# Performance work log

Hardware: AMD Instinct MI355X
Metric: run time of the kernel (lower is better)

The kernel has to match this reference:

```python
import jax, jax.numpy as jnp
import numpy as np

EMBED = 512
HEADS = 8
SCALE = 4
B, N = 2, 2048
DH = EMBED // HEADS
EPS = 1e-5


def _mha(q_in, k_in, v_in, wq, bq, wk, bk, wv, bv, wo, bo, causal):
    Bq, Nq, _ = q_in.shape
    Nk = k_in.shape[1]
    Q = (q_in @ wq + bq).reshape(Bq, Nq, HEADS, DH)
    K = (k_in @ wk + bk).reshape(Bq, Nk, HEADS, DH)
    V = (v_in @ wv + bv).reshape(Bq, Nk, HEADS, DH)
    # scores: [B, H, Nq, Nk]
    scores = jnp.einsum('bqhd,bkhd->bhqk', Q, K) / np.sqrt(DH).astype(np.float32)
    if causal:
        mask = jnp.triu(jnp.full((Nq, Nq), -jnp.inf, dtype=scores.dtype), k=1)
        scores = scores + mask[None, None]
    attn = jax.nn.softmax(scores, axis=-1)
    out = jnp.einsum('bhqk,bkhd->bqhd', attn, V).reshape(Bq, Nq, EMBED)
    return out @ wo + bo


def _ln(x, g, b):
    mu = jnp.mean(x, axis=-1, keepdims=True)
    var = jnp.var(x, axis=-1, keepdims=True)
    return (x - mu) * jax.lax.rsqrt(var + EPS) * g + b


def setup_inputs() -> dict:
    key = jax.random.key(0)
    ks = iter(jax.random.split(key, 32))
    p = lambda *s: 0.02 * jax.random.normal(next(ks), s, dtype=jnp.float32)
    inp = {
        'x': jax.random.normal(next(ks), (B, N, EMBED), dtype=jnp.float32),
        'encoder_output': jax.random.normal(next(ks), (B, N, EMBED), dtype=jnp.float32),
    }
    for pre in ('sa', 'ca'):
        inp[pre + '_wq'] = p(EMBED, EMBED); inp[pre + '_bq'] = jnp.zeros(EMBED)
        inp[pre + '_wk'] = p(EMBED, EMBED); inp[pre + '_bk'] = jnp.zeros(EMBED)
        inp[pre + '_wv'] = p(EMBED, EMBED); inp[pre + '_bv'] = jnp.zeros(EMBED)
        inp[pre + '_wo'] = p(EMBED, EMBED); inp[pre + '_bo'] = jnp.zeros(EMBED)
    for i in (1, 2, 3):
        inp[f'ln{i}_g'] = jnp.ones(EMBED); inp[f'ln{i}_b'] = jnp.zeros(EMBED)
    inp['ff_w1'] = p(EMBED, SCALE * EMBED); inp['ff_b1'] = jnp.zeros(SCALE * EMBED)
    inp['ff_w2'] = p(SCALE * EMBED, EMBED); inp['ff_b2'] = jnp.zeros(EMBED)
    return inp


def reference(x, encoder_output,
              sa_wq, sa_bq, sa_wk, sa_bk, sa_wv, sa_bv, sa_wo, sa_bo,
              ca_wq, ca_bq, ca_wk, ca_bk, ca_wv, ca_bv, ca_wo, ca_bo,
              ln1_g, ln1_b, ln2_g, ln2_b, ln3_g, ln3_b,
              ff_w1, ff_b1, ff_w2, ff_b2):
    x = _mha(x, x, x, sa_wq, sa_bq, sa_wk, sa_bk, sa_wv, sa_bv, sa_wo, sa_bo, True) + x
    x = _ln(x, ln1_g, ln1_b)
    x = _mha(x, encoder_output, encoder_output,
             ca_wq, ca_bq, ca_wk, ca_bk, ca_wv, ca_bv, ca_wo, ca_bo, False) + x
    x = _ln(x, ln2_g, ln2_b)
    h = jax.nn.gelu(x @ ff_w1 + ff_b1, approximate=False)
    x = h @ ff_w2 + ff_b2 + x
    return _ln(x, ln3_g, ln3_b)
```

## Files before the change

### kernel.cpp

```cpp
#include <hip/hip_runtime.h>
#include <hip/hip_bf16.h>

typedef __bf16 bf16x8 __attribute__((ext_vector_type(8)));
typedef float f32x4 __attribute__((ext_vector_type(4)));
typedef unsigned short u16;

#define EMB 512
#define FF 2048
#define MTOT 4096
#define SEQ 2048

__device__ __forceinline__ u16 f2b(float f) {
  return __builtin_bit_cast(u16, (__bf16)f);
}

__device__ __forceinline__ void gload16(const u16* g, u16* l) {
  __builtin_amdgcn_global_load_lds(
      (const __attribute__((address_space(1))) unsigned int*)g,
      (__attribute__((address_space(3))) unsigned int*)l, 16, 0, 0);
}

__global__ __launch_bounds__(256) void prep_all(
    const float* s0, const float* s1, const float* s2, const float* s3,
    const float* s4, const float* s5, const float* s6, const float* s7,
    const float* s8, const float* s9,
    u16* d0, u16* d1, u16* d2, u16* d3, u16* d4,
    u16* d5, u16* d6, u16* d7, u16* d8, u16* d9,
    const float* x, u16* xb, const float* enc, u16* encb,
    const float* bq1, const float* bk1, const float* bv1, float* bqkv,
    const float* bk2, const float* bv2, float* bkv) {
  int z = blockIdx.z, bx = blockIdx.x, by = blockIdx.y;
  int tid = threadIdx.x;
  if (z >= 10) {
    int fb = by * 64 + bx;
    const float* src = (z == 10) ? x : enc;
    u16* dst = (z == 10) ? xb : encb;
    size_t base = (size_t)fb * 2048 + tid * 8;
    float4 a = *(const float4*)(src + base);
    float4 b = *(const float4*)(src + base + 4);
    uint4 u;
    u.x = f2b(a.x) | ((unsigned)f2b(a.y) << 16);
    u.y = f2b(a.z) | ((unsigned)f2b(a.w) << 16);
    u.z = f2b(b.x) | ((unsigned)f2b(b.y) << 16);
    u.w = f2b(b.z) | ((unsigned)f2b(b.w) << 16);
    *(uint4*)(dst + base) = u;
    return;
  }
  if (z == 0 && bx == 16 && by == 0) {
    for (int i = tid; i < 1536; i += 256)
      bqkv[i] = (i < 512) ? bq1[i] : (i < 1024 ? bk1[i - 512] : bv1[i - 1024]);
    return;
  }
  if (z == 1 && bx == 16 && by == 0) {
    for (int i = tid; i < 1024; i += 256)
      bkv[i] = (i < 512) ? bk2[i] : bv2[i - 512];
    return;
  }
  const float* src; u16* dst; int K, N;
  switch (z) {
    case 0: src = s0; dst = d0; K = 512; N = 512; break;
    case 1: src = s1; dst = d1; K = 512; N = 512; break;
    case 2: src = s2; dst = d2; K = 512; N = 512; break;
    case 3: src = s3; dst = d3; K = 512; N = 512; break;
    case 4: src = s4; dst = d4; K = 512; N = 512; break;
    case 5: src = s5; dst = d5; K = 512; N = 512; break;
    case 6: src = s6; dst = d6; K = 512; N = 512; break;
    case 7: src = s7; dst = d7; K = 512; N = 512; break;
    case 8: src = s8; dst = d8; K = 512; N = 2048; break;
    default: src = s9; dst = d9; K = 2048; N = 512; break;
  }
  int ntl, ktl;
  if (z == 9) { ktl = bx; ntl = by; } else { ntl = bx; ktl = by; }
  if (ntl * 32 >= N || ktl * 32 >= K) return;
  __shared__ float t[32][33];
  int tx = tid & 31, ty = tid >> 5;
  int n0 = ntl * 32, k0 = ktl * 32;
#pragma unroll
  for (int i = 0; i < 4; i++)
    t[ty + i * 8][tx] = src[(size_t)(k0 + ty + i * 8) * N + n0 + tx];
  __syncthreads();
#pragma unroll
  for (int i = 0; i < 4; i++)
    dst[(size_t)(n0 + ty + i * 8) * K + k0 + tx] = f2b(t[tx][ty + i * 8]);
}

template <int BM, int BN, bool OUTB, bool OUTF, bool RES, bool GELU_>
__global__ __launch_bounds__(256) void gemm_bt(
    const u16* __restrict__ A, const u16* __restrict__ Bt,
    const float* __restrict__ bias, const float* __restrict__ resid,
    u16* __restrict__ outb, float* __restrict__ outf, int K, int Nd) {
  constexpr int MI = BM / 32;
  constexpr int NI = BN / 32;
  constexpr int RA = BM / 64;
  constexpr int RB = BN / 64;
  __shared__ u16 As[2][BM * 32];
  __shared__ u16 Bs[2][BN * 32];
  int tid = threadIdx.x;
  int lane = tid & 63, w = tid >> 6;
  int g = lane >> 4, li = lane & 15;
  int wr = w >> 1, wc = w & 1;
  int m0 = blockIdx.x * BM, n0 = blockIdx.y * BN;
  const u16* srcs[RA + RB];
  int ldsoff[RA + RB];
#pragma unroll
  for (int r = 0; r < RA + RB; r++) {
    int ca = (r < RA ? r * 256 : (r - RA) * 256) + tid;
    int row = ca >> 2, chv = ca & 3;
    int csw = chv ^ ((row ^ (row >> 2)) & 3);
    srcs[r] = (r < RA ? A + (size_t)(m0 + row) * K : Bt + (size_t)(n0 + row) * K) + csw * 8;
    ldsoff[r] = ((r < RA ? r * 256 : (r - RA) * 256) + w * 64) * 8;
  }
  int s2a = (li ^ (li >> 2)) & 3;
  f32x4 acc[MI][NI] = {};
  int T = K >> 5;
  auto stage = [&](int t, int buf) {
    int k0 = t << 5;
#pragma unroll
    for (int r = 0; r < RA; r++) gload16(srcs[r] + k0, &As[buf][ldsoff[r]]);
#pragma unroll
    for (int r = RA; r < RA + RB; r++) gload16(srcs[r] + k0, &Bs[buf][ldsoff[r]]);
  };
  stage(0, 0);
  __syncthreads();
  for (int t = 0; t < T; t++) {
    int cur = t & 1;
    if (t + 1 < T) stage(t + 1, cur ^ 1);
    bf16x8 af[MI], bfr[NI];
#pragma unroll
    for (int i = 0; i < MI; i++)
      af[i] = *(const bf16x8*)&As[cur][(wr * (BM / 2) + i * 16 + li) * 32 + (g ^ s2a) * 8];
#pragma unroll
    for (int i = 0; i < NI; i++)
      bfr[i] = *(const bf16x8*)&Bs[cur][(wc * (BN / 2) + i * 16 + li) * 32 + (g ^ s2a) * 8];
#pragma unroll
    for (int mi = 0; mi < MI; mi++)
#pragma unroll
      for (int ni = 0; ni < NI; ni++)
        acc[mi][ni] = __builtin_amdgcn_mfma_f32_16x16x32_bf16(af[mi], bfr[ni], acc[mi][ni], 0, 0, 0);
    __syncthreads();
  }
#pragma unroll
  for (int mi = 0; mi < MI; mi++)
#pragma unroll
    for (int ni = 0; ni < NI; ni++) {
      int gn = n0 + wc * (BN / 2) + ni * 16 + li;
      float bv = bias[gn];
#pragma unroll
      for (int r = 0; r < 4; r++) {
        int gm = m0 + wr * (BM / 2) + mi * 16 + g * 4 + r;
        float v = acc[mi][ni][r] + bv;
        if (RES) v += resid[(size_t)gm * Nd + gn];
        if (GELU_) v = 0.5f * v * (1.0f + erff(v * 0.70710678118654752f));
        if (OUTF) outf[(size_t)gm * Nd + gn] = v;
        if (OUTB) outb[(size_t)gm * Nd + gn] = f2b(v);
      }
    }
}

template <bool CAUSAL>
__global__ __launch_bounds__(256) void attn_fwd(
    const u16* __restrict__ Q, const u16* __restrict__ Kp,
    const u16* __restrict__ Vp, u16* __restrict__ O, int qs, int kvs) {
  __shared__ u16 Ks[2][128 * 64];
  __shared__ u16 Vt[2][64 * 128];
  __shared__ u16 Ps[4][16 * 128];
  int tid = threadIdx.x;
  int lane = tid & 63, w = tid >> 6;
  int g = lane >> 4, li = lane & 15;
  int idx = blockIdx.x;
  int bh = idx & 15;
  int qbi = idx >> 4;
  if (CAUSAL) qbi = (SEQ / 64 - 1) - qbi;
  int qb = qbi * 64;
  int b = bh >> 3, h = bh & 7;
  const u16* Qh = Q + (size_t)b * SEQ * qs + h * 64;
  const u16* Kh = Kp + (size_t)b * SEQ * kvs + h * 64;
  const u16* Vh = Vp + (size_t)b * SEQ * kvs + h * 64;
  int qrow = qb + w * 16 + li;
  bf16x8 qa[2];
#pragma unroll
  for (int ks = 0; ks < 2; ks++) {
    bf16x8 tq = *(const bf16x8*)&Qh[(size_t)qrow * qs + ks * 32 + g * 8];
#pragma unroll
    for (int j = 0; j < 8; j++) tq[j] = (__bf16)((float)tq[j] * 0.18033688011112042f);
    qa[ks] = tq;
  }
  int kcc = lane & 7;
  const u16* Ksrc[4];
#pragma unroll
  for (int j = 0; j < 4; j++) {
    int row = j * 32 + w * 8 + (lane >> 3);
    int sw = ((j * 4 + w) ^ (lane >> 3)) & 7;
    Ksrc[j] = Kh + (size_t)row * kvs + (kcc ^ sw) * 8;
  }
  size_t kstep = (size_t)128 * kvs;
  int kq = tid & 31, dcv = tid >> 5;
  const u16* Vsrc = Vh + (size_t)(4 * kq) * kvs + dcv * 8;
  uint4 vr[4];
  auto stageK = [&](int t, int buf) {
    size_t o = (size_t)t * kstep;
    u16* dst = &Ks[buf][w * 512];
#pragma unroll
    for (int j = 0; j < 4; j++) gload16(Ksrc[j] + o, dst + j * 2048);
  };
  auto loadV = [&](int t) {
    size_t o = (size_t)t * kstep;
#pragma unroll
    for (int kk = 0; kk < 4; kk++)
      vr[kk] = *(const uint4*)(Vsrc + o + (size_t)kk * kvs);
  };
  auto writeV = [&](int buf) {
    const u16* a0 = (const u16*)&vr[0];
    const u16* a1 = (const u16*)&vr[1];
    const u16* a2 = (const u16*)&vr[2];
    const u16* a3 = (const u16*)&vr[3];
#pragma unroll
    for (int jj = 0; jj < 8; jj++) {
      int d = dcv * 8 + jj;
      int swv = ((d >> 3) ^ d) & 15;
      uint2 pk;
      pk.x = (unsigned)a0[jj] | ((unsigned)a1[jj] << 16);
      pk.y = (unsigned)a2[jj] | ((unsigned)a3[jj] << 16);
      *(uint2*)&Vt[buf][d * 128 + ((kq >> 1) ^ swv) * 8 + 4 * (kq & 1)] = pk;
    }
  };
  int T = CAUSAL ? (qb >> 7) + 1 : SEQ / 128;
  stageK(0, 0);
  loadV(0);
  writeV(0);
  __syncthreads();
  f32x4 o[4] = {};
  float mreg = -1e30f, lreg = 0.f;
  for (int t = 0; t < T; t++) {
    int cur = t & 1;
    if (t + 1 < T) { stageK(t + 1, cur ^ 1); loadV(t + 1); }
    int kv0 = t << 7;
    f32x4 S[8] = {};
    __builtin_amdgcn_s_setprio(1);
#pragma unroll
    for (int nt = 0; nt < 8; nt++) {
      int krow = nt * 16 + li;
      int sw = ((krow >> 3) ^ krow) & 7;
#pragma unroll
      for (int ks = 0; ks < 2; ks++) {
        bf16x8 kb = *(const bf16x8*)&Ks[cur][krow * 64 + ((ks * 4 + g) ^ sw) * 8];
        S[nt] = __builtin_amdgcn_mfma_f32_16x16x32_bf16(kb, qa[ks], S[nt], 0, 0, 0);
      }
    }
    __builtin_amdgcn_s_setprio(0);
    if (CAUSAL && (kv0 + 127 > qb + w * 16)) {
#pragma unroll
      for (int nt = 0; nt < 8; nt++) {
        int kb0 = kv0 + nt * 16 + g * 4;
#pragma unroll
        for (int r = 0; r < 4; r++)
          if (kb0 + r > qrow) S[nt][r] = -1e30f;
      }
    }
    f32x4 mx = S[0];
#pragma unroll
    for (int nt = 1; nt < 8; nt++)
#pragma unroll
      for (int r = 0; r < 4; r++) mx[r] = fmaxf(mx[r], S[nt][r]);
    float pm = fmaxf(fmaxf(mx[0], mx[1]), fmaxf(mx[2], mx[3]));
    pm = fmaxf(pm, __shfl_xor(pm, 16, 64));
    pm = fmaxf(pm, __shfl_xor(pm, 32, 64));
    bool need = __any(pm > mreg + 8.0f);
    float nm = need ? fmaxf(mreg, pm) : mreg;
    f32x4 acc4 = {0.f, 0.f, 0.f, 0.f};
#pragma unroll
    for (int nt = 0; nt < 8; nt++)
#pragma unroll
      for (int r = 0; r < 4; r++) {
        float e = exp2f(S[nt][r] - nm);
        S[nt][r] = e;
        acc4[r] += e;
      }
    float rs = (acc4[0] + acc4[1]) + (acc4[2] + acc4[3]);
    rs += __shfl_xor(rs, 16, 64);
    rs += __shfl_xor(rs, 32, 64);
    if (need) {
      float csc = exp2f(mreg - nm);
      lreg = lreg * csc + rs;
      mreg = nm;
      float cscr[4];
#pragma unroll
      for (int r = 0; r < 4; r++)
        cscr[r] = __shfl(csc, (lane & 48) | (g * 4 + r), 64);
#pragma unroll
      for (int nd = 0; nd < 4; nd++)
#pragma unroll
        for (int r = 0; r < 4; r++) o[nd][r] *= cscr[r];
    } else {
      lreg += rs;
    }
#pragma unroll
    for (int nt = 0; nt < 8; nt++) {
      int cp = 2 * nt + (g >> 1);
      uint2 pk;
      pk.x = (unsigned)f2b(S[nt][0]) | ((unsigned)f2b(S[nt][1]) << 16);
      pk.y = (unsigned)f2b(S[nt][2]) | ((unsigned)f2b(S[nt][3]) << 16);
      *(uint2*)&Ps[w][li * 128 + ((cp ^ li) * 8) + 4 * (g & 1)] = pk;
    }
    bf16x8 pa[4];
#pragma unroll
    for (int k2 = 0; k2 < 4; k2++)
      pa[k2] = *(const bf16x8*)&Ps[w][li * 128 + (((k2 * 4 + g) ^ li) * 8)];
    __builtin_amdgcn_s_setprio(1);
#pragma unroll
    for (int nd = 0; nd < 4; nd++) {
      int d = nd * 16 + li;
      int swv = ((d >> 3) ^ d) & 15;
#pragma unroll
      for (int k2 = 0; k2 < 4; k2++) {
        bf16x8 vb = *(const bf16x8*)&Vt[cur][d * 128 + (((k2 * 4 + g) ^ swv) * 8)];
        o[nd] = __builtin_amdgcn_mfma_f32_16x16x32_bf16(pa[k2], vb, o[nd], 0, 0, 0);
      }
    }
    __builtin_amdgcn_s_setprio(0);
    if (t + 1 < T) writeV(cur ^ 1);
    __syncthreads();
  }
  float linv = 1.0f / lreg;
  float invr[4];
#pragma unroll
  for (int r = 0; r < 4; r++)
    invr[r] = __shfl(linv, (lane & 48) | (g * 4 + r), 64);
#pragma unroll
  for (int nd = 0; nd < 4; nd++)
#pragma unroll
    for (int r = 0; r < 4; r++)
      O[(size_t)b * SEQ * EMB + (size_t)(qb + w * 16 + g * 4 + r) * EMB + h * 64 + nd * 16 + li] =
          f2b(o[nd][r] * invr[r]);
}

__global__ __launch_bounds__(256) void ln_fused(
    const float* __restrict__ in, const float* __restrict__ gamma,
    const float* __restrict__ beta, float* __restrict__ outf, u16* __restrict__ outb) {
  int row = blockIdx.x * 4 + (threadIdx.x >> 6);
  int lane = threadIdx.x & 63;
  const float* p = in + (size_t)row * EMB + lane * 8;
  float v[8];
  *(float4*)&v[0] = *(const float4*)p;
  *(float4*)&v[4] = *(const float4*)(p + 4);
  float s = 0.f, q = 0.f;
#pragma unroll
  for (int j = 0; j < 8; j++) { s += v[j]; q += v[j] * v[j]; }
#pragma unroll
  for (int d = 1; d < 64; d <<= 1) {
    s += __shfl_xor(s, d, 64);
    q += __shfl_xor(q, d, 64);
  }
  float mu = s * (1.0f / EMB);
  float var = q * (1.0f / EMB) - mu * mu;
  float rsig = rsqrtf(var + 1e-5f);
  float gg[8], bb[8];
  *(float4*)&gg[0] = *(const float4*)(gamma + lane * 8);
  *(float4*)&gg[4] = *(const float4*)(gamma + lane * 8 + 4);
  *(float4*)&bb[0] = *(const float4*)(beta + lane * 8);
  *(float4*)&bb[4] = *(const float4*)(beta + lane * 8 + 4);
  float o[8];
#pragma unroll
  for (int j = 0; j < 8; j++) o[j] = (v[j] - mu) * rsig * gg[j] + bb[j];
  float* po = outf + (size_t)row * EMB + lane * 8;
  *(float4*)po = *(float4*)&o[0];
  *(float4*)(po + 4) = *(float4*)&o[4];
  if (outb) {
    uint4 u;
    u.x = f2b(o[0]) | ((unsigned)f2b(o[1]) << 16);
    u.y = f2b(o[2]) | ((unsigned)f2b(o[3]) << 16);
    u.z = f2b(o[4]) | ((unsigned)f2b(o[5]) << 16);
    u.w = f2b(o[6]) | ((unsigned)f2b(o[7]) << 16);
    *(uint4*)(outb + (size_t)row * EMB + lane * 8) = u;
  }
}

extern "C" void kernel_launch(void* const* d_in, const int* in_sizes, int n_in,
                              void* d_out, int out_size, void* d_ws, size_t ws_size,
                              hipStream_t stream) {
  const float* x     = (const float*)d_in[0];
  const float* enc   = (const float*)d_in[1];
  const float* sa_wq = (const float*)d_in[2];
  const float* sa_bq = (const float*)d_in[3];
  const float* sa_wk = (const float*)d_in[4];
  const float* sa_bk = (const float*)d_in[5];
  const float* sa_wv = (const float*)d_in[6];
  const float* sa_bv = (const float*)d_in[7];
  const float* sa_wo = (const float*)d_in[8];
  const float* sa_bo = (const float*)d_in[9];
  const float* ca_wq = (const float*)d_in[10];
  const float* ca_bq = (const float*)d_in[11];
  const float* ca_wk = (const float*)d_in[12];
  const float* ca_bk = (const float*)d_in[13];
  const float* ca_wv = (const float*)d_in[14];
  const float* ca_bv = (const float*)d_in[15];
  const float* ca_wo = (const float*)d_in[16];
  const float* ca_bo = (const float*)d_in[17];
  const float* ln1_g = (const float*)d_in[18];
  const float* ln1_b = (const float*)d_in[19];
  const float* ln2_g = (const float*)d_in[20];
  const float* ln2_b = (const float*)d_in[21];
  const float* ln3_g = (const float*)d_in[22];
  const float* ln3_b = (const float*)d_in[23];
  const float* ff_w1 = (const float*)d_in[24];
  const float* ff_b1 = (const float*)d_in[25];
  const float* ff_w2 = (const float*)d_in[26];
  const float* ff_b2 = (const float*)d_in[27];

  char* ws = (char*)d_ws;
  size_t off = 0;
  auto alloc = [&](size_t bytes) {
    void* p = ws + off;
    off = (off + bytes + 255) & ~(size_t)255;
    return p;
  };
  u16* qkvT_sa  = (u16*)alloc((size_t)1536 * EMB * 2);
  u16* oT_sa    = (u16*)alloc((size_t)EMB * EMB * 2);
  u16* qT_ca    = (u16*)alloc((size_t)EMB * EMB * 2);
  u16* kvT_ca   = (u16*)alloc((size_t)1024 * EMB * 2);
  u16* oT_ca    = (u16*)alloc((size_t)EMB * EMB * 2);
  u16* w1T      = (u16*)alloc((size_t)FF * EMB * 2);
  u16* w2T      = (u16*)alloc((size_t)EMB * FF * 2);
  float* bqkv_sa = (float*)alloc(1536 * 4);
  float* bkv_ca  = (float*)alloc(1024 * 4);
  u16* xb    = (u16*)alloc((size_t)MTOT * EMB * 2);
  u16* encb  = (u16*)alloc((size_t)MTOT * EMB * 2);
  u16* qkv   = (u16*)alloc((size_t)MTOT * 1536 * 2);
  u16* attnb = (u16*)alloc((size_t)MTOT * EMB * 2);
  float* t0  = (float*)alloc((size_t)MTOT * EMB * 4);
  float* x1  = (float*)alloc((size_t)MTOT * EMB * 4);
  u16* x1b   = (u16*)alloc((size_t)MTOT * EMB * 2);
  float* x2  = (float*)alloc((size_t)MTOT * EMB * 4);
  u16* x2b   = (u16*)alloc((size_t)MTOT * EMB * 2);
  u16* hbuf  = (u16*)alloc((size_t)MTOT * FF * 2);
  u16* qca  = xb;
  u16* kvca = qkv;

  prep_all<<<dim3(64, 16, 12), 256, 0, stream>>>(
      sa_wq, sa_wk, sa_wv, sa_wo, ca_wq, ca_wk, ca_wv, ca_wo, ff_w1, ff_w2,
      qkvT_sa, qkvT_sa + 512 * EMB, qkvT_sa + 1024 * EMB, oT_sa, qT_ca,
      kvT_ca, kvT_ca + 512 * EMB, oT_ca, w1T, w2T,
      x, xb, enc, encb,
      sa_bq, sa_bk, sa_bv, bqkv_sa, ca_bk, ca_bv, bkv_ca);

  gemm_bt<128, 64, true, false, false, false><<<dim3(32, 24), 256, 0, stream>>>(
      xb, qkvT_sa, bqkv_sa, nullptr, qkv, nullptr, EMB, 1536);
  attn_fwd<true><<<512, 256, 0, stream>>>(qkv, qkv + 512, qkv + 1024, attnb, 1536, 1536);
  gemm_bt<64, 64, false, true, true, false><<<dim3(64, 8), 256, 0, stream>>>(
      attnb, oT_sa, sa_bo, x, nullptr, t0, EMB, EMB);
  ln_fused<<<1024, 256, 0, stream>>>(t0, ln1_g, ln1_b, x1, x1b);

  gemm_bt<64, 64, true, false, false, false><<<dim3(64, 8), 256, 0, stream>>>(
      x1b, qT_ca, ca_bq, nullptr, qca, nullptr, EMB, EMB);
  gemm_bt<128, 64, true, false, false, false><<<dim3(32, 16), 256, 0, stream>>>(
      encb, kvT_ca, bkv_ca, nullptr, kvca, nullptr, EMB, 1024);
  attn_fwd<false><<<512, 256, 0, stream>>>(qca, kvca, kvca + 512, attnb, EMB, 1024);
  gemm_bt<64, 64, false, true, true, false><<<dim3(64, 8), 256, 0, stream>>>(
      attnb, oT_ca, ca_bo, x1, nullptr, t0, EMB, EMB);
  ln_fused<<<1024, 256, 0, stream>>>(t0, ln2_g, ln2_b, x2, x2b);

  gemm_bt<128, 128, true, false, false, true><<<dim3(32, 16), 256, 0, stream>>>(
      x2b, w1T, ff_b1, nullptr, hbuf, nullptr, EMB, FF);
  gemm_bt<64, 64, false, true, true, false><<<dim3(64, 8), 256, 0, stream>>>(
      hbuf, w2T, ff_b2, x2, nullptr, t0, FF, EMB);
  ln_fused<<<1024, 256, 0, stream>>>(t0, ln3_g, ln3_b, (float*)d_out, nullptr);
}
```

Measured before the change: 339.7 us.

## Deepen GEMM K-tile to 64 with vmcnt-based async prefetch pipeline

Doubles the GEMM K-step to 64 with an 8-chunk XOR swizzle. It replaces the syncthreads double-buffer with explicit vmcnt waits and raw barriers, so the stage for t+2 is issued after compute and overlaps the next iteration. The FFN1 GEMM tile also drops from 128x128 to 128x64 to launch more blocks. Shared memory per block grows, which may lower occupancy, and the hand-written waitcnt logic assumes a fixed count of loads per stage.

```diff
diff --git a/kernel.cpp b/kernel.cpp
--- a/kernel.cpp
+++ b/kernel.cpp
@@ -18,6 +18,14 @@
   __builtin_amdgcn_global_load_lds(
       (const __attribute__((address_space(1))) unsigned int*)g,
       (__attribute__((address_space(3))) unsigned int*)l, 16, 0, 0);
+}
+
+template <int N>
+__device__ __forceinline__ void wait_vmcnt() {
+  if constexpr (N == 0) asm volatile("s_waitcnt vmcnt(0)" ::: "memory");
+  else if constexpr (N == 4) asm volatile("s_waitcnt vmcnt(4)" ::: "memory");
+  else if constexpr (N == 6) asm volatile("s_waitcnt vmcnt(6)" ::: "memory");
+  else if constexpr (N == 8) asm volatile("s_waitcnt vmcnt(8)" ::: "memory");
 }
 
 __global__ __launch_bounds__(256) void prep_all(
@@ -91,53 +99,67 @@
     u16* __restrict__ outb, float* __restrict__ outf, int K, int Nd) {
   constexpr int MI = BM / 32;
   constexpr int NI = BN / 32;
-  constexpr int RA = BM / 64;
-  constexpr int RB = BN / 64;
-  __shared__ u16 As[2][BM * 32];
-  __shared__ u16 Bs[2][BN * 32];
+  constexpr int RA = BM / 32;
+  constexpr int RB = BN / 32;
+  constexpr int L = RA + RB;
+  __shared__ u16 As[2][BM * 64];
+  __shared__ u16 Bs[2][BN * 64];
   int tid = threadIdx.x;
   int lane = tid & 63, w = tid >> 6;
   int g = lane >> 4, li = lane & 15;
   int wr = w >> 1, wc = w & 1;
   int m0 = blockIdx.x * BM, n0 = blockIdx.y * BN;
-  const u16* srcs[RA + RB];
-  int ldsoff[RA + RB];
-#pragma unroll
-  for (int r = 0; r < RA + RB; r++) {
-    int ca = (r < RA ? r * 256 : (r - RA) * 256) + tid;
-    int row = ca >> 2, chv = ca & 3;
-    int csw = chv ^ ((row ^ (row >> 2)) & 3);
-    srcs[r] = (r < RA ? A + (size_t)(m0 + row) * K : Bt + (size_t)(n0 + row) * K) + csw * 8;
-    ldsoff[r] = ((r < RA ? r * 256 : (r - RA) * 256) + w * 64) * 8;
-  }
-  int s2a = (li ^ (li >> 2)) & 3;
+  int row_s = tid >> 3, ch_s = tid & 7;
+  const u16* srcs[L];
+  int ldsoff[L];
+#pragma unroll
+  for (int r = 0; r < L; r++) {
+    int rr = (r < RA) ? r : r - RA;
+    int row = rr * 32 + row_s;
+    int csw = ch_s ^ (row & 7);
+    srcs[r] = ((r < RA) ? A + (size_t)(m0 + row) * K : Bt + (size_t)(n0 + row) * K) + csw * 8;
+    ldsoff[r] = (rr * 256 + tid) * 8;
+  }
   f32x4 acc[MI][NI] = {};
-  int T = K >> 5;
+  int T = K >> 6;
   auto stage = [&](int t, int buf) {
-    int k0 = t << 5;
+    int k0 = t << 6;
 #pragma unroll
     for (int r = 0; r < RA; r++) gload16(srcs[r] + k0, &As[buf][ldsoff[r]]);
 #pragma unroll
-    for (int r = RA; r < RA + RB; r++) gload16(srcs[r] + k0, &Bs[buf][ldsoff[r]]);
+    for (int r = RA; r < L; r++) gload16(srcs[r] + k0, &Bs[buf][ldsoff[r]]);
   };
   stage(0, 0);
-  __syncthreads();
+  stage(1, 1);
   for (int t = 0; t < T; t++) {
     int cur = t & 1;
-    if (t + 1 < T) stage(t + 1, cur ^ 1);
-    bf16x8 af[MI], bfr[NI];
-#pragma unroll
-    for (int i = 0; i < MI; i++)
-      af[i] = *(const bf16x8*)&As[cur][(wr * (BM / 2) + i * 16 + li) * 32 + (g ^ s2a) * 8];
-#pragma unroll
-    for (int i = 0; i < NI; i++)
-      bfr[i] = *(const bf16x8*)&Bs[cur][(wc * (BN / 2) + i * 16 + li) * 32 + (g ^ s2a) * 8];
+    if (t == T - 1) wait_vmcnt<0>(); else wait_vmcnt<L>();
+    __builtin_amdgcn_s_barrier();
+    __builtin_amdgcn_sched_barrier(0);
+    bf16x8 af[MI][2], bfr[NI][2];
+#pragma unroll
+    for (int i = 0; i < MI; i++) {
+      int R = wr * (BM / 2) + i * 16 + li;
+#pragma unroll
+      for (int ks = 0; ks < 2; ks++)
+        af[i][ks] = *(const bf16x8*)&As[cur][R * 64 + (((ks * 4 + g) ^ (R & 7)) * 8)];
+    }
+#pragma unroll
+    for (int i = 0; i < NI; i++) {
+      int R = wc * (BN / 2) + i * 16 + li;
+#pragma unroll
+      for (int ks = 0; ks < 2; ks++)
+        bfr[i][ks] = *(const bf16x8*)&Bs[cur][R * 64 + (((ks * 4 + g) ^ (R & 7)) * 8)];
+    }
 #pragma unroll
     for (int mi = 0; mi < MI; mi++)
 #pragma unroll
       for (int ni = 0; ni < NI; ni++)
-        acc[mi][ni] = __builtin_amdgcn_mfma_f32_16x16x32_bf16(af[mi], bfr[ni], acc[mi][ni], 0, 0, 0);
-    __syncthreads();
+#pragma unroll
+        for (int ks = 0; ks < 2; ks++)
+          acc[mi][ni] = __builtin_amdgcn_mfma_f32_16x16x32_bf16(af[mi][ks], bfr[ni][ks], acc[mi][ni], 0, 0, 0);
+    __builtin_amdgcn_s_barrier();
+    if (t + 2 < T) stage(t + 2, cur);
   }
 #pragma unroll
   for (int mi = 0; mi < MI; mi++)
@@ -459,7 +481,7 @@
       attnb, oT_ca, ca_bo, x1, nullptr, t0, EMB, EMB);
   ln_fused<<<1024, 256, 0, stream>>>(t0, ln2_g, ln2_b, x2, x2b);
 
-  gemm_bt<128, 128, true, false, false, true><<<dim3(32, 16), 256, 0, stream>>>(
+  gemm_bt<128, 64, true, false, false, true><<<dim3(32, 32), 256, 0, stream>>>(
       x2b, w1T, ff_b1, nullptr, hbuf, nullptr, EMB, FF);
   gemm_bt<64, 64, false, true, true, false><<<dim3(64, 8), 256, 0, stream>>>(
       hbuf, w2T, ff_b2, x2, nullptr, t0, FF, EMB);
```

Result: faster. 325.7 us (-4.1%).
